# Performance work log

Hardware: AMD Instinct MI355X
Metric: run time of the kernel (lower is better)

## Reference

```python
import jax, jax.numpy as jnp
import numpy as np
import math

B, S, D = 1, 2048, 1024
H = 16
DH = D // H
FF = 4096
NPOS = 128
MLPW = 32
EPS = 1e-5


def setup_inputs() -> dict:
    key = jax.random.key(0)
    ks = jax.random.split(key, 16)
    sd = lambda n: 1.0 / math.sqrt(n)
    return {
        "x": jax.random.normal(ks[0], (B, S, D), jnp.float32),
        "wq": jax.random.normal(ks[1], (D, D), jnp.float32) * sd(D),
        "wk": jax.random.normal(ks[2], (D, D), jnp.float32) * sd(D),
        "wv": jax.random.normal(ks[3], (D, D), jnp.float32) * sd(D),
        "wo": jax.random.normal(ks[4], (D, D), jnp.float32) * sd(D),
        "pos_emb": jax.random.normal(ks[5], (DH, NPOS), jnp.float32) * 0.02,
        "mlp_w1": jax.random.normal(ks[6], (2 * H, MLPW), jnp.float32) * sd(2 * H),
        "mlp_b1": jnp.zeros((MLPW,), jnp.float32),
        "mlp_w2": jax.random.normal(ks[7], (MLPW, H), jnp.float32) * sd(MLPW),
        "mlp_b2": jnp.zeros((H,), jnp.float32),
        "ffn_w1": jax.random.normal(ks[8], (D, FF), jnp.float32) * sd(D),
        "ffn_w2": jax.random.normal(ks[9], (FF, D), jnp.float32) * sd(FF),
        "ffn_w3": jax.random.normal(ks[10], (D, FF), jnp.float32) * sd(D),
        "attn_norm_w": jnp.ones((D,), jnp.float32),
        "ffn_norm_w": jnp.ones((D,), jnp.float32),
    }


def _rmsnorm(x, w):
    xf = x.astype(jnp.float32)
    n = xf * jax.lax.rsqrt(jnp.mean(xf * xf, axis=-1, keepdims=True) + EPS)
    return w * n.astype(x.dtype)


def reference(x, wq, wk, wv, wo, pos_emb, mlp_w1, mlp_b1, mlp_w2, mlp_b2,
              ffn_w1, ffn_w2, ffn_w3, attn_norm_w, ffn_norm_w):
    # ---- attention branch ----
    nx = _rmsnorm(x, attn_norm_w)
    split = lambda t: t.reshape(B, S, H, DH).transpose(0, 2, 1, 3)  # b h s d
    q = split(nx @ wq)
    k = split(nx @ wk)
    v = split(nx @ wv)
    scores = jnp.einsum('bhsd,bhtd->bhst', q, k) / math.sqrt(DH)  # [B,H,S,S]

    # ---- CoPE-style dynamic contextual bias ----
    gates = jax.nn.sigmoid(scores)
    # reversed cumulative sum over key axis
    pos = jnp.flip(jnp.cumsum(jnp.flip(gates, -1), axis=-1), -1)
    pos = jnp.minimum(pos, NPOS - 1)
    pos_floor = jnp.floor(pos).astype(jnp.int32)
    pos_ceil = jnp.ceil(pos).astype(jnp.int32)
    logits_int = jnp.einsum('bhsd,dn->bhsn', q, pos_emb)  # [B,H,S,NPOS]
    logits_ceil = jnp.take_along_axis(logits_int, pos_ceil, axis=-1)
    logits_floor = jnp.take_along_axis(logits_int, pos_floor, axis=-1)
    w = pos - pos_floor.astype(pos.dtype)
    cope_bias = logits_ceil * w + logits_floor * (1.0 - w)  # [B,H,S,S]

    # per-(b,s1,s2) tiny MLP over concat(scores, cope_bias) along head axis
    combined = jnp.concatenate(
        (scores.transpose(0, 2, 3, 1), cope_bias.transpose(0, 2, 3, 1)), axis=-1)  # [B,S,S,2H]
    hmid = jax.nn.silu(combined @ mlp_w1 + mlp_b1)
    dyn_bias = (hmid @ mlp_w2 + mlp_b2).transpose(0, 3, 1, 2)  # [B,H,S,S]

    attn = jax.nn.softmax(scores + dyn_bias, axis=-1)
    out = jnp.einsum('bhst,bhtd->bhsd', attn, v)
    out = out.transpose(0, 2, 1, 3).reshape(B, S, D) @ wo
    x = x + out

    # ---- SwiGLU FFN branch ----
    nx = _rmsnorm(x, ffn_norm_w)
    ff = (jax.nn.silu(nx @ ffn_w1) * (nx @ ffn_w3)) @ ffn_w2
    return x + ff
```

## Files before the change

### kernel.cpp

```cpp
#include <hip/hip_runtime.h>
#include <hip/hip_bf16.h>
#include <hip/hip_fp16.h>
#include <math.h>

#define SEQ 2048
#define DMODEL 1024
#define NH 16
#define DHEAD 64
#define FFDIM 4096
#define NPOSE 128
#define MLPWID 32
#define EPSV 1e-5f
#define CHUNK 1024
#define NCH (SEQ / CHUNK)

typedef unsigned short ushort_t;
typedef unsigned int uint_t;
typedef _Float16 f16;
typedef __attribute__((ext_vector_type(8))) _Float16 f16x8;
typedef __attribute__((ext_vector_type(4))) float f32x4;

union HF8 { f16x8 v; f16 h[8]; ushort_t s[8]; uint2 u2[2]; uint4 u4; };
union U1H2 { uint_t u; f16 h[2]; };
union U2H4 { uint2 u; f16 h[4]; };

__device__ __forceinline__ float sigm(float x) {
    return __builtin_amdgcn_rcpf(1.0f + __expf(-x));
}
__device__ __forceinline__ void gl_lds16(const void* g, void* l) {
    __builtin_amdgcn_global_load_lds((const __attribute__((address_space(1))) uint_t*)g,
                                     (__attribute__((address_space(3))) uint_t*)l, 16, 0, 0);
}

__global__ __launch_bounds__(256) void rmsnormf_k(const float* __restrict__ x,
                                                  const float* __restrict__ w,
                                                  f16* __restrict__ o) {
    int row = blockIdx.x;
    int tid = threadIdx.x;
    const float4* xr = (const float4*)(x + (size_t)row * DMODEL);
    float4 v = xr[tid];
    float ss = v.x * v.x + v.y * v.y + v.z * v.z + v.w * v.w;
#pragma unroll
    for (int d = 1; d < 64; d <<= 1) ss += __shfl_xor(ss, d, 64);
    __shared__ float red[4];
    int lane = tid & 63, wv = tid >> 6;
    if (lane == 0) red[wv] = ss;
    __syncthreads();
    float tot = red[0] + red[1] + red[2] + red[3];
    float r = rsqrtf(tot / (float)DMODEL + EPSV);
    const float4* wr = (const float4*)w;
    float4 wv4 = wr[tid];
    U2H4 ob;
    ob.h[0] = (f16)(v.x * r * wv4.x);
    ob.h[1] = (f16)(v.y * r * wv4.y);
    ob.h[2] = (f16)(v.z * r * wv4.z);
    ob.h[3] = (f16)(v.w * r * wv4.w);
    ((uint2*)(o + (size_t)row * DMODEL))[tid] = ob.u;
}

__global__ __launch_bounds__(256) void tv_k(const ushort_t* __restrict__ vb,
                                            ushort_t* __restrict__ vt) {
    int h = blockIdx.y, t0 = blockIdx.x * 64;
    __shared__ ushort_t T[64][76];
    int tid = threadIdx.x;
#pragma unroll
    for (int it = 0; it < 2; it++) {
        int a = tid + it * 256;
        int t = a >> 3, c8 = (a & 7) * 8;
        HF8 v;
        v.u4 = *(const uint4*)(vb + (size_t)(t0 + t) * DMODEL + h * 64 + c8);
#pragma unroll
        for (int j = 0; j < 8; j++) T[c8 + j][t] = v.s[j];
    }
    __syncthreads();
#pragma unroll
    for (int it = 0; it < 2; it++) {
        int a = tid + it * 256;
        int d = a >> 3, c8 = (a & 7) * 8;
        HF8 o;
#pragma unroll
        for (int j = 0; j < 8; j++) o.s[j] = T[d][c8 + j];
        *(uint4*)(vt + ((size_t)h * 64 + d) * SEQ + t0 + c8) = o.u4;
    }
}

__global__ __launch_bounds__(256) void transconv_k(const float* __restrict__ in,
                                                   f16* __restrict__ out,
                                                   int K, int N) {
    __shared__ f16 T[64][72];
    int k0 = blockIdx.y * 64, n0 = blockIdx.x * 64;
    int tid = threadIdx.x;
    int r = tid >> 4, c4 = (tid & 15) * 4;
#pragma unroll
    for (int i = 0; i < 4; i++) {
        float4 v = *(const float4*)(in + (size_t)(k0 + r + i * 16) * N + n0 + c4);
        T[c4 + 0][r + i * 16] = (f16)v.x;
        T[c4 + 1][r + i * 16] = (f16)v.y;
        T[c4 + 2][r + i * 16] = (f16)v.z;
        T[c4 + 3][r + i * 16] = (f16)v.w;
    }
    __syncthreads();
    int n = tid >> 2, kk = (tid & 3) * 16;
    uint4* dst = (uint4*)(out + (size_t)(n0 + n) * K + k0 + kk);
    dst[0] = *(const uint4*)&T[n][kk];
    dst[1] = *(const uint4*)&T[n][kk + 8];
}

__global__ __launch_bounds__(256) void transconv2_k(const float* __restrict__ w1,
                                                    const float* __restrict__ w3,
                                                    f16* __restrict__ out,
                                                    int K, int N) {
    __shared__ f16 T[64][72];
    int k0 = blockIdx.y * 64, n0 = blockIdx.x * 64;
    int tid = threadIdx.x;
    int r = tid >> 4, c4 = (tid & 15) * 4;
    int n = tid >> 2, kk = (tid & 3) * 16;
#pragma unroll
    for (int half = 0; half < 2; half++) {
        const float* in = half ? w3 : w1;
#pragma unroll
        for (int i = 0; i < 4; i++) {
            float4 v = *(const float4*)(in + (size_t)(k0 + r + i * 16) * N + n0 + c4);
            T[c4 + 0][r + i * 16] = (f16)v.x;
            T[c4 + 1][r + i * 16] = (f16)v.y;
            T[c4 + 2][r + i * 16] = (f16)v.z;
            T[c4 + 3][r + i * 16] = (f16)v.w;
        }
        __syncthreads();
        int gc = n0 + n;
        int rp = (gc >> 4) * 32 + (gc & 15) + half * 16;
        uint4* dst = (uint4*)(out + (size_t)rp * K + k0 + kk);
        dst[0] = *(const uint4*)&T[n][kk];
        dst[1] = *(const uint4*)&T[n][kk + 8];
        __syncthreads();
    }
}

__global__ __launch_bounds__(256) void gemm128_k(const f16* __restrict__ A,
                                                 const f16* __restrict__ Bt,
                                                 const float* __restrict__ add,
                                                 void* __restrict__ Cout,
                                                 int M, int N, int K, int mode) {
    __shared__ f16 Al[128 * 32];
    __shared__ f16 Bl[128 * 32];
    int tid = threadIdx.x;
    int lane = tid & 63, wave = tid >> 6;
    int gx = gridDim.x, gy = gridDim.y;
    int nwg = gx * gy;
    int bx = blockIdx.x, by = blockIdx.y;
    if ((nwg & 7) == 0) {
        int flat = by * gx + bx;
        int cpx = nwg >> 3;
        int l = (flat & 7) * cpx + (flat >> 3);
        bx = l / gy;
        by = l % gy;
    }
    int brow = by * 128, bcol = bx * 128;
    int wr = (wave >> 1) * 64, wc = (wave & 1) * 64;
    f32x4 acc[4][4];
#pragma unroll
    for (int m = 0; m < 4; m++)
#pragma unroll
        for (int n = 0; n < 4; n++) acc[m][n] = (f32x4){0.f, 0.f, 0.f, 0.f};

    const f16* Ag = A + (size_t)(brow + (tid >> 2)) * K + (tid & 3) * 8;
    const f16* Bg = Bt + (size_t)(bcol + (tid >> 2)) * K + (tid & 3) * 8;
    f16* Ald = &Al[wave * 512];
    f16* Bld = &Bl[wave * 512];
    size_t rstep = (size_t)64 * K;

    for (int k0 = 0; k0 < K; k0 += 32) {
        gl_lds16(Ag + k0, Ald);
        gl_lds16(Ag + k0 + rstep, Ald + 2048);
        gl_lds16(Bg + k0, Bld);
        gl_lds16(Bg + k0 + rstep, Bld + 2048);
        __syncthreads();
        f16x8 af[4], bfr[4];
        int arow = wr + (lane & 15);
        int brw = wc + (lane & 15);
        int kof = (lane >> 4) * 8;
#pragma unroll
        for (int m = 0; m < 4; m++) af[m] = *(const f16x8*)&Al[(arow + m * 16) * 32 + kof];
#pragma unroll
        for (int n = 0; n < 4; n++) bfr[n] = *(const f16x8*)&Bl[(brw + n * 16) * 32 + kof];
#pragma unroll
        for (int m = 0; m < 4; m++)
#pragma unroll
            for (int n = 0; n < 4; n++)
                acc[m][n] = __builtin_amdgcn_mfma_f32_16x16x32_f16(af[m], bfr[n], acc[m][n], 0, 0, 0);
        __syncthreads();
    }
    int crow0 = brow + wr + (lane >> 4) * 4;
    int ccol = bcol + wc + (lane & 15);
#pragma unroll
    for (int m = 0; m < 4; m++)
#pragma unroll
        for (int j = 0; j < 4; j++) {
            int row = crow0 + m * 16 + j;
            if (mode == 4) {
#pragma unroll
                for (int n = 0; n < 4; n += 2) {
                    int c = ccol + n * 16;
                    int colOut = (c >> 5) * 16 + (c & 15);
                    float v1 = acc[m][n][j];
                    float v3 = acc[m][n + 1][j];
                    ((f16*)Cout)[(size_t)row * (N / 2) + colOut] =
                        (f16)(v1 * sigm(v1) * v3);
                }
            } else {
#pragma unroll
                for (int n = 0; n < 4; n++) {
                    int col = ccol + n * 16;
                    float v = acc[m][n][j];
                    if (mode == 0) {
                        if (add) v += add[(size_t)row * N + col];
                        ((float*)Cout)[(size_t)row * N + col] = v;
                    } else {
                        ((f16*)Cout)[(size_t)row * N + col] = (f16)v;
                    }
                }
            }
        }
}

__global__ __launch_bounds__(256) void gemm64_k(const f16* __restrict__ A,
                                                const f16* __restrict__ Bt,
                                                const float* __restrict__ add,
                                                void* __restrict__ Cout,
                                                int M, int N, int K, int mode,
                                                f16* __restrict__ p2,
                                                f16* __restrict__ p3) {
    __shared__ f16 Al[64 * 32];
    __shared__ f16 Bl[64 * 32];
    int tid = threadIdx.x;
    int lane = tid & 63, wave = tid >> 6;
    int gx = gridDim.x, gy = gridDim.y;
    int nwg = gx * gy;
    int bx = blockIdx.x, by = blockIdx.y;
    if ((nwg & 7) == 0) {
        int flat = by * gx + bx;
        int cpx = nwg >> 3;
        int l = (flat & 7) * cpx + (flat >> 3);
        bx = l / gy;
        by = l % gy;
    }
    int brow = by * 64, bcol = bx * 64;
    int wr = (wave >> 1) * 32, wc = (wave & 1) * 32;
    f32x4 acc[2][2];
#pragma unroll
    for (int m = 0; m < 2; m++)
#pragma unroll
        for (int n = 0; n < 2; n++) acc[m][n] = (f32x4){0.f, 0.f, 0.f, 0.f};

    const f16* Ag = A + (size_t)(brow + (tid >> 2)) * K + (tid & 3) * 8;
    const f16* Bg = Bt + (size_t)(bcol + (tid >> 2)) * K + (tid & 3) * 8;
    f16* Ald = &Al[wave * 512];
    f16* Bld = &Bl[wave * 512];

    for (int k0 = 0; k0 < K; k0 += 32) {
        gl_lds16(Ag + k0, Ald);
        gl_lds16(Bg + k0, Bld);
        __syncthreads();
        f16x8 af[2], bfr[2];
        int kof = (lane >> 4) * 8;
#pragma unroll
        for (int m = 0; m < 2; m++)
            af[m] = *(const f16x8*)&Al[(wr + m * 16 + (lane & 15)) * 32 + kof];
#pragma unroll
        for (int n = 0; n < 2; n++)
            bfr[n] = *(const f16x8*)&Bl[(wc + n * 16 + (lane & 15)) * 32 + kof];
#pragma unroll
        for (int m = 0; m < 2; m++)
#pragma unroll
            for (int n = 0; n < 2; n++)
                acc[m][n] = __builtin_amdgcn_mfma_f32_16x16x32_f16(af[m], bfr[n], acc[m][n], 0, 0, 0);
        __syncthreads();
    }
    int crow0 = brow + wr + (lane >> 4) * 4;
    int ccol = bcol + wc + (lane & 15);
#pragma unroll
    for (int m = 0; m < 2; m++)
#pragma unroll
        for (int j = 0; j < 4; j++) {
            int row = crow0 + m * 16 + j;
#pragma unroll
            for (int n = 0; n < 2; n++) {
                int col = ccol + n * 16;
                float v = acc[m][n][j];
                if (mode == 0) {
                    if (add) v += add[(size_t)row * N + col];
                    ((float*)Cout)[(size_t)row * N + col] = v;
                } else if (mode == 1) {
                    ((f16*)Cout)[(size_t)row * N + col] = (f16)v;
                } else {
                    size_t o = (size_t)row * DMODEL;
                    if (col < DMODEL) ((f16*)Cout)[o + col] = (f16)v;
                    else if (col < 2 * DMODEL) p2[o + col - DMODEL] = (f16)v;
                    else p3[o + col - 2 * DMODEL] = (f16)v;
                }
            }
        }
}

__global__ __launch_bounds__(256) void scoresm_k(const f16* __restrict__ qf,
                                                 const f16* __restrict__ kf,
                                                 f16* __restrict__ sc, int cb) {
    int h = blockIdx.z;
    int il0 = blockIdx.y * 64;
    int j0 = blockIdx.x * 64;
    __shared__ f16 Qf[64][72];
    __shared__ f16 Kf[64][72];
    int tid = threadIdx.x;
    {
        int r = tid >> 2, c0 = (tid & 3) * 16;
        const f16* p;
        p = qf + (size_t)(cb + il0 + r) * DMODEL + h * 64 + c0;
        *(uint4*)&Qf[r][c0] = *(const uint4*)p;
        *(uint4*)&Qf[r][c0 + 8] = *(const uint4*)(p + 8);
        p = kf + (size_t)(j0 + r) * DMODEL + h * 64 + c0;
        *(uint4*)&Kf[r][c0] = *(const uint4*)p;
        *(uint4*)&Kf[r][c0 + 8] = *(const uint4*)(p + 8);
    }
    __syncthreads();
    int lane = tid & 63, wave = tid >> 6;
    int wr = (wave >> 1) * 32, wc = (wave & 1) * 32;
    f32x4 acc[2][2];
#pragma unroll
    for (int m = 0; m < 2; m++)
#pragma unroll
        for (int n = 0; n < 2; n++) acc[m][n] = (f32x4){0.f, 0.f, 0.f, 0.f};
#pragma unroll
    for (int ks = 0; ks < 2; ks++) {
        int kof = ks * 32 + (lane >> 4) * 8;
        f16x8 aQ[2], bK[2];
#pragma unroll
        for (int m = 0; m < 2; m++)
            aQ[m] = *(const f16x8*)&Qf[wr + m * 16 + (lane & 15)][kof];
#pragma unroll
        for (int n = 0; n < 2; n++)
            bK[n] = *(const f16x8*)&Kf[wc + n * 16 + (lane & 15)][kof];
#pragma unroll
        for (int m = 0; m < 2; m++)
#pragma unroll
            for (int n = 0; n < 2; n++)
                acc[m][n] = __builtin_amdgcn_mfma_f32_16x16x32_f16(aQ[m], bK[n], acc[m][n], 0, 0, 0);
    }
#pragma unroll
    for (int m = 0; m < 2; m++)
#pragma unroll
        for (int j = 0; j < 4; j++) {
            int il = il0 + wr + m * 16 + (lane >> 4) * 4 + j;
#pragma unroll
            for (int n = 0; n < 2; n++) {
                int jj = j0 + wc + n * 16 + (lane & 15);
                sc[((size_t)h * CHUNK + il) * SEQ + jj] = (f16)(acc[m][n][j] * 0.125f);
            }
        }
}

__global__ __launch_bounds__(256) void copelogits_k(const f16* __restrict__ qf,
                                                    const float* __restrict__ pe,
                                                    f16* __restrict__ li) {
    int s1 = blockIdx.x;
    int tid = threadIdx.x;
    __shared__ float PE[DHEAD * NPOSE];
    __shared__ float QR[DMODEL];
    for (int i = tid; i < DHEAD * NPOSE; i += 256) PE[i] = pe[i];
    for (int i = tid; i < DMODEL; i += 256) QR[i] = (float)qf[(size_t)s1 * DMODEL + i];
    __syncthreads();
#pragma unroll
    for (int j = 0; j < 8; j++) {
        int o = j * 256 + tid;
        int h = o >> 7, n = o & 127;
        const float* qhp = &QR[h * DHEAD];
        float acc = 0.0f;
#pragma unroll 8
        for (int d = 0; d < DHEAD; d++) acc += qhp[d] * PE[d * NPOSE + n];
        li[(size_t)s1 * (NH * NPOSE) + o] = (f16)acc;
    }
}

#define CSTR 2052
__global__ __launch_bounds__(1024, 1) void cope_k(f16* __restrict__ sc,
                                                  const f16* __restrict__ li,
                                                  const float* __restrict__ w1,
                                                  const float* __restrict__ b1,
                                                  const float* __restrict__ w2,
                                                  const float* __restrict__ b2,
                                                  int cb) {
    __shared__ f16 C[32 * CSTR];
    __shared__ uint_t Lif2[NH * 130];
    __shared__ f16 HMB[16][16 * 36];
    int r = blockIdx.x;
    int tid = threadIdx.x;
    int lane = tid & 63, wv = tid >> 6;

    const f16* srow = sc + ((size_t)wv * CHUNK + r) * SEQ;
    HF8 rv[4];
#pragma unroll
    for (int c = 0; c < 4; c++) rv[c].u4 = *(const uint4*)&srow[c * 512 + lane * 8];

    {
        const f16* lh = li + (size_t)(cb + r) * (NH * NPOSE) + wv * NPOSE;
#pragma unroll
        for (int e = 0; e < 2; e++) {
            int n = lane + e * 64;
            U1H2 pk;
            pk.h[0] = lh[n];
            pk.h[1] = lh[(n < NPOSE - 1) ? n + 1 : NPOSE - 1];
            Lif2[wv * 130 + n] = pk.u;
        }
    }

    {
        f16* crow = &C[wv * CSTR];
        f16* brow = &C[(16 + wv) * CSTR];
        const uint_t* lrow = &Lif2[wv * 130];
        float carry = 0.0f;
        for (int c = 3; c >= 0; c--) {
            HF8 sv = rv[c];
            float g[8];
            float S = 0.0f;
#pragma unroll
            for (int e = 0; e < 8; e++) {
                g[e] = sigm((float)sv.h[e]);
                S += g[e];
            }
#pragma unroll
            for (int dd = 1; dd < 64; dd <<= 1) {
                float o = __shfl_down(S, dd, 64);
                S = (lane + dd < 64) ? S + o : S;
            }
            float total = __shfl(S, 0, 64);
            float p = S + carry;
            carry += total;
            HF8 bo;
#pragma unroll
            for (int e = 0; e < 8; e++) {
                float pos = fminf(p, 127.0f);
                int fl = (int)pos;
                float fr = pos - (float)fl;
                U1H2 lv;
                lv.u = lrow[fl];
                float lf = (float)lv.h[0];
                bo.h[e] = (f16)(lf + ((float)lv.h[1] - lf) * fr);
                p -= g[e];
            }
            int t = c * 512 + lane * 8;
            *(uint4*)&crow[t] = sv.u4;
            *(uint4*)&brow[t] = bo.u4;
        }
    }
    __syncthreads();

    int fkg = lane >> 4;
    int fc = lane & 15;
    HF8 w1f[2], w2f;
    float b1v[2], b2v;
#pragma unroll
    for (int half = 0; half < 2; half++) {
#pragma unroll
        for (int j = 0; j < 8; j++)
            w1f[half].h[j] = (f16)w1[(fkg * 8 + j) * MLPWID + half * 16 + fc];
        b1v[half] = b1[half * 16 + fc];
    }
#pragma unroll
    for (int j = 0; j < 8; j++) w2f.h[j] = (f16)w2[(fkg * 8 + j) * NH + fc];
    b2v = b2[fc];

    f16* hmb = HMB[wv];
    for (int tt = wv; tt < SEQ / 16; tt += 16) {
        int t0 = tt * 16;
        HF8 af;
#pragma unroll
        for (int j = 0; j < 8; j++) af.h[j] = C[(fkg * 8 + j) * CSTR + t0 + fc];
        f32x4 acc0 = (f32x4){b1v[0], b1v[0], b1v[0], b1v[0]};
        f32x4 acc1 = (f32x4){b1v[1], b1v[1], b1v[1], b1v[1]};
        acc0 = __builtin_amdgcn_mfma_f32_16x16x32_f16(af.v, w1f[0].v, acc0, 0, 0, 0);
        acc1 = __builtin_amdgcn_mfma_f32_16x16x32_f16(af.v, w1f[1].v, acc1, 0, 0, 0);
#pragma unroll
        for (int j2 = 0; j2 < 4; j2++) {
            int p = fkg * 4 + j2;
            float h0 = acc0[j2]; h0 = h0 * sigm(h0);
            float h1 = acc1[j2]; h1 = h1 * sigm(h1);
            hmb[p * 36 + fc] = (f16)h0;
            hmb[p * 36 + 16 + fc] = (f16)h1;
        }
        HF8 hf;
        hf.u2[0] = *(const uint2*)&hmb[fc * 36 + fkg * 8];
        hf.u2[1] = *(const uint2*)&hmb[fc * 36 + fkg * 8 + 4];
        f32x4 acc2 = (f32x4){b2v, b2v, b2v, b2v};
        acc2 = __builtin_amdgcn_mfma_f32_16x16x32_f16(hf.v, w2f.v, acc2, 0, 0, 0);
#pragma unroll
        for (int j2 = 0; j2 < 4; j2 += 2) {
            uint_t* pp = (uint_t*)&C[fc * CSTR + t0 + fkg * 4 + j2];
            U1H2 old, neu;
            old.u = *pp;
            neu.h[0] = (f16)((float)old.h[0] + acc2[j2]);
            neu.h[1] = (f16)((float)old.h[1] + acc2[j2 + 1]);
            *pp = neu.u;
        }
    }
    __syncthreads();

    {
        const f16* row = &C[wv * CSTR];
        float vals[32];
        float m = -1e30f;
#pragma unroll
        for (int c = 0; c < 4; c++) {
            HF8 sv;
            sv.u4 = *(const uint4*)&row[c * 512 + lane * 8];
#pragma unroll
            for (int e = 0; e < 8; e++) {
                vals[c * 8 + e] = (float)sv.h[e];
                m = fmaxf(m, vals[c * 8 + e]);
            }
        }
#pragma unroll
        for (int d = 1; d < 64; d <<= 1) m = fmaxf(m, __shfl_xor(m, d, 64));
        float s = 0.0f;
#pragma unroll
        for (int c = 0; c < 32; c++) {
            vals[c] = __expf(vals[c] - m);
            s += vals[c];
        }
#pragma unroll
        for (int d = 1; d < 64; d <<= 1) s += __shfl_xor(s, d, 64);
        float ri = __builtin_amdgcn_rcpf(s);
        f16* dst = sc + ((size_t)wv * CHUNK + r) * SEQ;
#pragma unroll
        for (int c = 0; c < 4; c++) {
            HF8 po;
#pragma unroll
            for (int e = 0; e < 8; e++) po.h[e] = (f16)(vals[c * 8 + e] * ri);
            *(uint4*)&dst[c * 512 + lane * 8] = po.u4;
        }
    }
}

__global__ __launch_bounds__(256) void pvm_k(const f16* __restrict__ scP,
                                             const ushort_t* __restrict__ vt,
                                             f16* __restrict__ aob, int cb) {
    int h = blockIdx.y;
    int s0 = blockIdx.x * 32;
    __shared__ f16 P[32][72];
    __shared__ f16 Vt[64][72];
    int tid = threadIdx.x;
    int lane = tid & 63, wave = tid >> 6;
    int wr = (wave >> 1) * 16, wc = (wave & 1) * 32;
    f32x4 acc[2];
    acc[0] = (f32x4){0.f, 0.f, 0.f, 0.f};
    acc[1] = (f32x4){0.f, 0.f, 0.f, 0.f};
    int pr = tid >> 3, pc = (tid & 7) * 8;
    int vr = tid >> 2, vc = (tid & 3) * 16;
    for (int t0 = 0; t0 < SEQ; t0 += 64) {
        {
            *(uint4*)&P[pr][pc] =
                *(const uint4*)(scP + ((size_t)h * CHUNK + s0 + pr) * SEQ + t0 + pc);
            const ushort_t* vp = vt + ((size_t)h * 64 + vr) * SEQ + t0 + vc;
            *(uint4*)&Vt[vr][vc] = *(const uint4*)vp;
            *(uint4*)&Vt[vr][vc + 8] = *(const uint4*)(vp + 8);
        }
        __syncthreads();
#pragma unroll
        for (int ks = 0; ks < 2; ks++) {
            int kof = ks * 32 + (lane >> 4) * 8;
            f16x8 pa = *(const f16x8*)&P[wr + (lane & 15)][kof];
#pragma unroll
            for (int n = 0; n < 2; n++) {
                f16x8 vb = *(const f16x8*)&Vt[wc + n * 16 + (lane & 15)][kof];
                acc[n] = __builtin_amdgcn_mfma_f32_16x16x32_f16(pa, vb, acc[n], 0, 0, 0);
            }
        }
        __syncthreads();
    }
#pragma unroll
    for (int j = 0; j < 4; j++) {
        int s = cb + s0 + wr + (lane >> 4) * 4 + j;
#pragma unroll
        for (int n = 0; n < 2; n++) {
            int d = h * 64 + wc + n * 16 + (lane & 15);
            aob[(size_t)s * DMODEL + d] = (f16)acc[n][j];
        }
    }
}

extern "C" void kernel_launch(void* const* d_in, const int* in_sizes, int n_in,
                              void* d_out, int out_size, void* d_ws, size_t ws_size,
                              hipStream_t stream) {
    const float* x = (const float*)d_in[0];
    const float* wq = (const float*)d_in[1];
    const float* wk = (const float*)d_in[2];
    const float* wv = (const float*)d_in[3];
    const float* wo = (const float*)d_in[4];
    const float* pos_emb = (const float*)d_in[5];
    const float* mlp_w1 = (const float*)d_in[6];
    const float* mlp_b1 = (const float*)d_in[7];
    const float* mlp_w2 = (const float*)d_in[8];
    const float* mlp_b2 = (const float*)d_in[9];
    const float* ffn_w1 = (const float*)d_in[10];
    const float* ffn_w2 = (const float*)d_in[11];
    const float* ffn_w3 = (const float*)d_in[12];
    const float* attn_norm_w = (const float*)d_in[13];
    const float* ffn_norm_w = (const float*)d_in[14];
    float* out = (float*)d_out;

    char* ws = (char*)d_ws;
    const size_t MB = 1024 * 1024;
    f16* nxb = (f16*)(ws + 0);
    f16* qf = (f16*)(ws + 4 * MB);
    f16* kf = (f16*)(ws + 8 * MB);
    f16* vb = (f16*)(ws + 12 * MB);
    f16* vt = (f16*)(ws + 16 * MB);
    f16* li = (f16*)(ws + 20 * MB);
    f16* aob = (f16*)(ws + 28 * MB);
    float* x1 = (float*)(ws + 32 * MB);
    f16* wqkvt = (f16*)(ws + 40 * MB);
    f16* sc = (f16*)(ws + 40 * MB);
    f16* wot = (f16*)(ws + 40 * MB);
    f16* w13t = (f16*)(ws + 40 * MB);
    f16* w2t = (f16*)(ws + 56 * MB);
    f16* nxb2 = (f16*)(ws + 4 * MB);
    f16* g1b = (f16*)(ws + 8 * MB);

    transconv_k<<<dim3(DMODEL / 64, DMODEL / 64), 256, 0, stream>>>(wq, wqkvt, DMODEL, DMODEL);
    transconv_k<<<dim3(DMODEL / 64, DMODEL / 64), 256, 0, stream>>>(wk, wqkvt + 1024 * 1024, DMODEL, DMODEL);
    transconv_k<<<dim3(DMODEL / 64, DMODEL / 64), 256, 0, stream>>>(wv, wqkvt + 2 * 1024 * 1024, DMODEL, DMODEL);
    rmsnormf_k<<<SEQ, 256, 0, stream>>>(x, attn_norm_w, nxb);
    gemm64_k<<<dim3(3 * DMODEL / 64, SEQ / 64), 256, 0, stream>>>(
        nxb, wqkvt, nullptr, qf, SEQ, 3 * DMODEL, DMODEL, 2, kf, vb);
    copelogits_k<<<SEQ, 256, 0, stream>>>(qf, pos_emb, li);
    tv_k<<<dim3(SEQ / 64, NH), 256, 0, stream>>>((const ushort_t*)vb, (ushort_t*)vt);

    for (int ch = 0; ch < NCH; ch++) {
        int cb = ch * CHUNK;
        scoresm_k<<<dim3(SEQ / 64, CHUNK / 64, NH), 256, 0, stream>>>(qf, kf, sc, cb);
        cope_k<<<CHUNK, 1024, 0, stream>>>(sc, li, mlp_w1, mlp_b1, mlp_w2, mlp_b2, cb);
        pvm_k<<<dim3(CHUNK / 32, NH), 256, 0, stream>>>(sc, (const ushort_t*)vt, aob, cb);
    }

    transconv_k<<<dim3(DMODEL / 64, DMODEL / 64), 256, 0, stream>>>(wo, wot, DMODEL, DMODEL);
    gemm64_k<<<dim3(DMODEL / 64, SEQ / 64), 256, 0, stream>>>(
        aob, wot, x, x1, SEQ, DMODEL, DMODEL, 0, nullptr, nullptr);

    rmsnormf_k<<<SEQ, 256, 0, stream>>>(x1, ffn_norm_w, nxb2);
    transconv2_k<<<dim3(FFDIM / 64, DMODEL / 64), 256, 0, stream>>>(ffn_w1, ffn_w3, w13t, DMODEL, FFDIM);
    transconv_k<<<dim3(DMODEL / 64, FFDIM / 64), 256, 0, stream>>>(ffn_w2, w2t, FFDIM, DMODEL);
    gemm128_k<<<dim3(2 * FFDIM / 128, SEQ / 128), 256, 0, stream>>>(
        nxb2, w13t, nullptr, g1b, SEQ, 2 * FFDIM, DMODEL, 4);
    gemm64_k<<<dim3(DMODEL / 64, SEQ / 64), 256, 0, stream>>>(
        g1b, w2t, x1, out, SEQ, DMODEL, FFDIM, 0, nullptr, nullptr);
}
```

Measured before the change: 446.6 us.

## Replace 64x64 GEMMs with 128x128 tiles and split-K plus reduce

Removes the 64x64 GEMM kernel and routes the QKV, output-projection and FFN down-projection GEMMs through the 128x128 MFMA kernel. The output projection uses a 2-way split-K and the down projection a 4-way split-K, writing fp32 partials that a new reduce kernel sums together with the residual. Larger tiles give more data reuse per block, and split-K keeps enough blocks in flight for the narrow N=1024 outputs. The cost is extra fp32 partial-buffer traffic and one additional launch per split GEMM.

```diff
diff --git a/kernel.cpp b/kernel.cpp
--- a/kernel.cpp
+++ b/kernel.cpp
@@ -140,7 +140,10 @@
                                                  const f16* __restrict__ Bt,
                                                  const float* __restrict__ add,
                                                  void* __restrict__ Cout,
-                                                 int M, int N, int K, int mode) {
+                                                 int M, int N, int K, int mode,
+                                                 int Klen,
+                                                 f16* __restrict__ p2,
+                                                 f16* __restrict__ p3) {
     __shared__ f16 Al[128 * 32];
     __shared__ f16 Bl[128 * 32];
     int tid = threadIdx.x;
@@ -148,6 +151,7 @@
     int gx = gridDim.x, gy = gridDim.y;
     int nwg = gx * gy;
     int bx = blockIdx.x, by = blockIdx.y;
+    int bz = blockIdx.z;
     if ((nwg & 7) == 0) {
         int flat = by * gx + bx;
         int cpx = nwg >> 3;
@@ -163,13 +167,14 @@
 #pragma unroll
         for (int n = 0; n < 4; n++) acc[m][n] = (f32x4){0.f, 0.f, 0.f, 0.f};
 
-    const f16* Ag = A + (size_t)(brow + (tid >> 2)) * K + (tid & 3) * 8;
-    const f16* Bg = Bt + (size_t)(bcol + (tid >> 2)) * K + (tid & 3) * 8;
+    int kbase = bz * Klen;
+    const f16* Ag = A + (size_t)(brow + (tid >> 2)) * K + kbase + (tid & 3) * 8;
+    const f16* Bg = Bt + (size_t)(bcol + (tid >> 2)) * K + kbase + (tid & 3) * 8;
     f16* Ald = &Al[wave * 512];
     f16* Bld = &Bl[wave * 512];
     size_t rstep = (size_t)64 * K;
 
-    for (int k0 = 0; k0 < K; k0 += 32) {
+    for (int k0 = 0; k0 < Klen; k0 += 32) {
         gl_lds16(Ag + k0, Ald);
         gl_lds16(Ag + k0 + rstep, Ald + 2048);
         gl_lds16(Bg + k0, Bld);
@@ -215,91 +220,33 @@
                     if (mode == 0) {
                         if (add) v += add[(size_t)row * N + col];
                         ((float*)Cout)[(size_t)row * N + col] = v;
+                    } else if (mode == 1) {
+                        ((f16*)Cout)[(size_t)row * N + col] = (f16)v;
+                    } else if (mode == 2) {
+                        size_t o = (size_t)row * DMODEL;
+                        if (col < DMODEL) ((f16*)Cout)[o + col] = (f16)v;
+                        else if (col < 2 * DMODEL) p2[o + col - DMODEL] = (f16)v;
+                        else p3[o + col - 2 * DMODEL] = (f16)v;
                     } else {
-                        ((f16*)Cout)[(size_t)row * N + col] = (f16)v;
+                        ((float*)Cout)[(size_t)bz * M * N + (size_t)row * N + col] = v;
                     }
                 }
             }
         }
 }
 
-__global__ __launch_bounds__(256) void gemm64_k(const f16* __restrict__ A,
-                                                const f16* __restrict__ Bt,
+__global__ __launch_bounds__(256) void reduce_k(const float* __restrict__ parts,
+                                                int nz, size_t zstride,
                                                 const float* __restrict__ add,
-                                                void* __restrict__ Cout,
-                                                int M, int N, int K, int mode,
-                                                f16* __restrict__ p2,
-                                                f16* __restrict__ p3) {
-    __shared__ f16 Al[64 * 32];
-    __shared__ f16 Bl[64 * 32];
-    int tid = threadIdx.x;
-    int lane = tid & 63, wave = tid >> 6;
-    int gx = gridDim.x, gy = gridDim.y;
-    int nwg = gx * gy;
-    int bx = blockIdx.x, by = blockIdx.y;
-    if ((nwg & 7) == 0) {
-        int flat = by * gx + bx;
-        int cpx = nwg >> 3;
-        int l = (flat & 7) * cpx + (flat >> 3);
-        bx = l / gy;
-        by = l % gy;
-    }
-    int brow = by * 64, bcol = bx * 64;
-    int wr = (wave >> 1) * 32, wc = (wave & 1) * 32;
-    f32x4 acc[2][2];
-#pragma unroll
-    for (int m = 0; m < 2; m++)
-#pragma unroll
-        for (int n = 0; n < 2; n++) acc[m][n] = (f32x4){0.f, 0.f, 0.f, 0.f};
-
-    const f16* Ag = A + (size_t)(brow + (tid >> 2)) * K + (tid & 3) * 8;
-    const f16* Bg = Bt + (size_t)(bcol + (tid >> 2)) * K + (tid & 3) * 8;
-    f16* Ald = &Al[wave * 512];
-    f16* Bld = &Bl[wave * 512];
-
-    for (int k0 = 0; k0 < K; k0 += 32) {
-        gl_lds16(Ag + k0, Ald);
-        gl_lds16(Bg + k0, Bld);
-        __syncthreads();
-        f16x8 af[2], bfr[2];
-        int kof = (lane >> 4) * 8;
-#pragma unroll
-        for (int m = 0; m < 2; m++)
-            af[m] = *(const f16x8*)&Al[(wr + m * 16 + (lane & 15)) * 32 + kof];
-#pragma unroll
-        for (int n = 0; n < 2; n++)
-            bfr[n] = *(const f16x8*)&Bl[(wc + n * 16 + (lane & 15)) * 32 + kof];
-#pragma unroll
-        for (int m = 0; m < 2; m++)
-#pragma unroll
-            for (int n = 0; n < 2; n++)
-                acc[m][n] = __builtin_amdgcn_mfma_f32_16x16x32_f16(af[m], bfr[n], acc[m][n], 0, 0, 0);
-        __syncthreads();
-    }
-    int crow0 = brow + wr + (lane >> 4) * 4;
-    int ccol = bcol + wc + (lane & 15);
-#pragma unroll
-    for (int m = 0; m < 2; m++)
-#pragma unroll
-        for (int j = 0; j < 4; j++) {
-            int row = crow0 + m * 16 + j;
-#pragma unroll
-            for (int n = 0; n < 2; n++) {
-                int col = ccol + n * 16;
-                float v = acc[m][n][j];
-                if (mode == 0) {
-                    if (add) v += add[(size_t)row * N + col];
-                    ((float*)Cout)[(size_t)row * N + col] = v;
-                } else if (mode == 1) {
-                    ((f16*)Cout)[(size_t)row * N + col] = (f16)v;
-                } else {
-                    size_t o = (size_t)row * DMODEL;
-                    if (col < DMODEL) ((f16*)Cout)[o + col] = (f16)v;
-                    else if (col < 2 * DMODEL) p2[o + col - DMODEL] = (f16)v;
-                    else p3[o + col - 2 * DMODEL] = (f16)v;
-                }
-            }
-        }
+                                                float* __restrict__ out, int n4) {
+    int i = blockIdx.x * 256 + threadIdx.x;
+    if (i >= n4) return;
+    float4 s = ((const float4*)add)[i];
+    for (int z = 0; z < nz; z++) {
+        float4 p = *(const float4*)(parts + z * zstride + (size_t)i * 4);
+        s.x += p.x; s.y += p.y; s.z += p.z; s.w += p.w;
+    }
+    ((float4*)out)[i] = s;
 }
 
 __global__ __launch_bounds__(256) void scoresm_k(const f16* __restrict__ qf,
@@ -619,17 +566,21 @@
     f16* wqkvt = (f16*)(ws + 40 * MB);
     f16* sc = (f16*)(ws + 40 * MB);
     f16* wot = (f16*)(ws + 40 * MB);
+    float* partB = (float*)(ws + 42 * MB);
     f16* w13t = (f16*)(ws + 40 * MB);
     f16* w2t = (f16*)(ws + 56 * MB);
+    float* partC = (float*)(ws + 64 * MB);
     f16* nxb2 = (f16*)(ws + 4 * MB);
     f16* g1b = (f16*)(ws + 8 * MB);
+
+    const int N4 = SEQ * DMODEL / 4;
 
     transconv_k<<<dim3(DMODEL / 64, DMODEL / 64), 256, 0, stream>>>(wq, wqkvt, DMODEL, DMODEL);
     transconv_k<<<dim3(DMODEL / 64, DMODEL / 64), 256, 0, stream>>>(wk, wqkvt + 1024 * 1024, DMODEL, DMODEL);
     transconv_k<<<dim3(DMODEL / 64, DMODEL / 64), 256, 0, stream>>>(wv, wqkvt + 2 * 1024 * 1024, DMODEL, DMODEL);
     rmsnormf_k<<<SEQ, 256, 0, stream>>>(x, attn_norm_w, nxb);
-    gemm64_k<<<dim3(3 * DMODEL / 64, SEQ / 64), 256, 0, stream>>>(
-        nxb, wqkvt, nullptr, qf, SEQ, 3 * DMODEL, DMODEL, 2, kf, vb);
+    gemm128_k<<<dim3(3 * DMODEL / 128, SEQ / 128), 256, 0, stream>>>(
+        nxb, wqkvt, nullptr, qf, SEQ, 3 * DMODEL, DMODEL, 2, DMODEL, kf, vb);
     copelogits_k<<<SEQ, 256, 0, stream>>>(qf, pos_emb, li);
     tv_k<<<dim3(SEQ / 64, NH), 256, 0, stream>>>((const ushort_t*)vb, (ushort_t*)vt);
 
@@ -641,14 +592,16 @@
     }
 
     transconv_k<<<dim3(DMODEL / 64, DMODEL / 64), 256, 0, stream>>>(wo, wot, DMODEL, DMODEL);
-    gemm64_k<<<dim3(DMODEL / 64, SEQ / 64), 256, 0, stream>>>(
-        aob, wot, x, x1, SEQ, DMODEL, DMODEL, 0, nullptr, nullptr);
+    gemm128_k<<<dim3(DMODEL / 128, SEQ / 128, 2), 256, 0, stream>>>(
+        aob, wot, nullptr, partB, SEQ, DMODEL, DMODEL, 5, DMODEL / 2, nullptr, nullptr);
+    reduce_k<<<(N4 + 255) / 256, 256, 0, stream>>>(partB, 2, (size_t)SEQ * DMODEL, x, x1, N4);
 
     rmsnormf_k<<<SEQ, 256, 0, stream>>>(x1, ffn_norm_w, nxb2);
     transconv2_k<<<dim3(FFDIM / 64, DMODEL / 64), 256, 0, stream>>>(ffn_w1, ffn_w3, w13t, DMODEL, FFDIM);
     transconv_k<<<dim3(DMODEL / 64, FFDIM / 64), 256, 0, stream>>>(ffn_w2, w2t, FFDIM, DMODEL);
     gemm128_k<<<dim3(2 * FFDIM / 128, SEQ / 128), 256, 0, stream>>>(
-        nxb2, w13t, nullptr, g1b, SEQ, 2 * FFDIM, DMODEL, 4);
-    gemm64_k<<<dim3(DMODEL / 64, SEQ / 64), 256, 0, stream>>>(
-        g1b, w2t, x1, out, SEQ, DMODEL, FFDIM, 0, nullptr, nullptr);
-}
+        nxb2, w13t, nullptr, g1b, SEQ, 2 * FFDIM, DMODEL, 4, DMODEL, nullptr, nullptr);
+    gemm128_k<<<dim3(DMODEL / 128, SEQ / 128, 4), 256, 0, stream>>>(
+        g1b, w2t, nullptr, partC, SEQ, DMODEL, FFDIM, 5, FFDIM / 4, nullptr, nullptr);
+    reduce_k<<<(N4 + 255) / 256, 256, 0, stream>>>(partC, 4, (size_t)SEQ * DMODEL, x1, out, N4);
+}
```

Result: slower. 459.7 us (+2.9%).
